# Kernel tuning notes

Hardware: AMD Instinct MI355X
Metric: run time of the kernel (lower is better)

The kernel has to match this reference:

```python
import jax, jax.numpy as jnp
import numpy as np

B, S, D_MODEL, D_Q = 16, 2048, 384, 64


def setup_inputs() -> dict:
    key = jax.random.key(0)
    k1, k2, k3, k4 = jax.random.split(key, 4)
    x = jax.random.normal(k1, (B, S, D_MODEL), dtype=jnp.float32)
    # nn.Linear(d_model, d_q, bias=False) weights, stored as [d_model, d_q] so q = x @ Wq
    scale = 1.0 / np.sqrt(D_MODEL)
    Wq = jax.random.normal(k2, (D_MODEL, D_Q), dtype=jnp.float32) * scale
    Wk = jax.random.normal(k3, (D_MODEL, D_Q), dtype=jnp.float32) * scale
    Wv = jax.random.normal(k4, (D_MODEL, D_Q), dtype=jnp.float32) * scale
    return {"x": x, "Wq": Wq, "Wk": Wk, "Wv": Wv}


def reference(x, Wq, Wk, Wv):
    # x: [B, S, d_model]
    q = jnp.einsum("bsd,de->bse", x, Wq)  # [B, S, d_q]
    k = jnp.einsum("bsd,de->bse", x, Wk)
    v = jnp.einsum("bsd,de->bse", x, Wv)
    d_q = q.shape[-1]
    # full S x S score matrix, scaled by sqrt(d_q) as in the torch code (k.size(-1)**0.5)
    scores = jnp.einsum("bse,bte->bst", q, k) / jnp.sqrt(jnp.float32(d_q))
    s = x.shape[1]
    causal = jnp.tril(jnp.ones((s, s), dtype=bool))  # [S, S]
    scores = jnp.where(causal, scores, jnp.float32(-jnp.inf))
    probs = jax.nn.softmax(scores, axis=-1)
    # dropout is identity in eval/reference mode
    out = jnp.einsum("bst,bte->bse", probs, v)  # [B, S, d_q]
    return out
```

## Files before the change

kernel.cpp:

```cpp
#include <hip/hip_runtime.h>
#include <hip/hip_bf16.h>
#include <math.h>

#define BB 16
#define SS 2048
#define DM 384
#define DQ 64
#define M_ROWS (BB * SS)

typedef short short8 __attribute__((ext_vector_type(8)));
typedef float f32x4  __attribute__((ext_vector_type(4)));
typedef unsigned u32x4 __attribute__((ext_vector_type(4)));

#define WT_OFF 0
#define QB_OFF 73728
#define KB_OFF (QB_OFF + M_ROWS * DQ)
#define VT_OFF (KB_OFF + M_ROWS * DQ)

#define QSCALE 0.18033688011112042f

__device__ __forceinline__ short f2bf(float f) {
  unsigned u = __builtin_bit_cast(unsigned, f);
  unsigned r = (u + 0x7fffu + ((u >> 16) & 1u)) >> 16;
  return (short)r;
}
__device__ __forceinline__ unsigned cvtpk(float a, float b) {
  unsigned r;
  asm("v_cvt_pk_bf16_f32 %0, %1, %2" : "=v"(r) : "v"(a), "v"(b));
  return r;
}
__device__ __forceinline__ void async16(const short* g, short* l) {
  __builtin_amdgcn_global_load_lds(
      (const __attribute__((address_space(1))) unsigned int*)g,
      (__attribute__((address_space(3))) unsigned int*)l, 16, 0, 0);
}

__global__ void prep_w_kernel(const float* __restrict__ Wq,
                              const float* __restrict__ Wk,
                              const float* __restrict__ Wv,
                              short* __restrict__ ws) {
  int o = blockIdx.x * 256 + threadIdx.x;
  int mat = o / (DM * DQ);
  int r = o % (DM * DQ);
  int k = r / DQ, n = r % DQ;
  const float* W = (mat == 0) ? Wq : (mat == 1) ? Wk : Wv;
  ws[WT_OFF + mat * (DM * DQ) + n * DM + k] = f2bf(W[k * DQ + n]);
}

__global__ __launch_bounds__(256) void qkv_proj_mfma(
    const float* __restrict__ x, const short* __restrict__ ws_r,
    short* __restrict__ ws_w) {
  __shared__ short smem[2 * 192 * 64];
  short* Ep = smem;
  const int tid = threadIdx.x;
  const int lane = tid & 63, w = tid >> 6;
  const int cidx = lane & 15, g = lane >> 4;
  const int g8 = g * 8, g4 = g * 4;
  const int sw7 = cidx & 7;
  const int rows0 = blockIdx.x * 64;
  const short* Wt = ws_r + WT_OFF;

  f32x4 acc[12];
  #pragma unroll
  for (int i = 0; i < 12; ++i) acc[i] = (f32x4){0.f, 0.f, 0.f, 0.f};

  const float* xr = x + (size_t)(rows0 + 16 * w + cidx) * DM;

  #pragma unroll
  for (int it = 0; it < 6; ++it) {
    int i = it * 256 + tid;
    int row = i >> 3, gr = i & 7;
    const short* src = Wt + row * DM + ((gr ^ (row & 7)) * 8);
    async16(src, &smem[(it * 256 + w * 64) * 8]);
  }
  float4 xc0 = *(const float4*)(xr + g8);
  float4 xc1 = *(const float4*)(xr + g8 + 4);
  float4 xc2 = *(const float4*)(xr + 32 + g8);
  float4 xc3 = *(const float4*)(xr + 32 + g8 + 4);

  for (int ki = 0; ki < 6; ++ki) {
    __syncthreads();
    const short* cur = smem + (ki & 1) * 12288;

    if (ki < 5) {
      short* nxt = smem + ((ki + 1) & 1) * 12288;
      const int kn = (ki + 1) * 64;
      #pragma unroll
      for (int it = 0; it < 6; ++it) {
        int i = it * 256 + tid;
        int row = i >> 3, gr = i & 7;
        const short* src = Wt + row * DM + kn + ((gr ^ (row & 7)) * 8);
        async16(src, &nxt[(it * 256 + w * 64) * 8]);
      }
    }

    u32x4 ua, ub;
    ua[0] = cvtpk(xc0.x, xc0.y); ua[1] = cvtpk(xc0.z, xc0.w);
    ua[2] = cvtpk(xc1.x, xc1.y); ua[3] = cvtpk(xc1.z, xc1.w);
    ub[0] = cvtpk(xc2.x, xc2.y); ub[1] = cvtpk(xc2.z, xc2.w);
    ub[2] = cvtpk(xc3.x, xc3.y); ub[3] = cvtpk(xc3.z, xc3.w);
    short8 a0 = __builtin_bit_cast(short8, ua);
    short8 a1 = __builtin_bit_cast(short8, ub);

    if (ki < 5) {
      const float* xn = xr + (ki + 1) * 64;
      xc0 = *(const float4*)(xn + g8);
      xc1 = *(const float4*)(xn + g8 + 4);
      xc2 = *(const float4*)(xn + 32 + g8);
      xc3 = *(const float4*)(xn + 32 + g8 + 4);
    }

    #pragma unroll
    for (int ct = 0; ct < 12; ++ct) {
      int row = ct * 16 + cidx;
      short8 b0 = *(const short8*)&cur[row * 64 + ((g ^ sw7) * 8)];
      short8 b1 = *(const short8*)&cur[row * 64 + (((g + 4) ^ sw7) * 8)];
      acc[ct] = __builtin_amdgcn_mfma_f32_16x16x32_bf16(a0, b0, acc[ct], 0, 0, 0);
      acc[ct] = __builtin_amdgcn_mfma_f32_16x16x32_bf16(a1, b1, acc[ct], 0, 0, 0);
    }
  }

  __syncthreads();
  const int erow = 16 * w + g4;
  #pragma unroll
  for (int ct = 0; ct < 4; ++ct) {
    unsigned q01 = cvtpk(acc[ct][0] * QSCALE, acc[ct][1] * QSCALE);
    unsigned q23 = cvtpk(acc[ct][2] * QSCALE, acc[ct][3] * QSCALE);
    unsigned k01 = cvtpk(acc[4 + ct][0], acc[4 + ct][1]);
    unsigned k23 = cvtpk(acc[4 + ct][2], acc[4 + ct][3]);
    unsigned v01 = cvtpk(acc[8 + ct][0], acc[8 + ct][1]);
    unsigned v23 = cvtpk(acc[8 + ct][2], acc[8 + ct][3]);
    Ep[(erow + 0) * 200 + ct * 16 + cidx] = (short)q01;
    Ep[(erow + 1) * 200 + ct * 16 + cidx] = (short)(q01 >> 16);
    Ep[(erow + 2) * 200 + ct * 16 + cidx] = (short)q23;
    Ep[(erow + 3) * 200 + ct * 16 + cidx] = (short)(q23 >> 16);
    Ep[(erow + 0) * 200 + 64 + ct * 16 + cidx] = (short)k01;
    Ep[(erow + 1) * 200 + 64 + ct * 16 + cidx] = (short)(k01 >> 16);
    Ep[(erow + 2) * 200 + 64 + ct * 16 + cidx] = (short)k23;
    Ep[(erow + 3) * 200 + 64 + ct * 16 + cidx] = (short)(k23 >> 16);
    Ep[(ct * 16 + cidx) * 200 + 128 + erow + 0] = (short)v01;
    Ep[(ct * 16 + cidx) * 200 + 128 + erow + 1] = (short)(v01 >> 16);
    Ep[(ct * 16 + cidx) * 200 + 128 + erow + 2] = (short)v23;
    Ep[(ct * 16 + cidx) * 200 + 128 + erow + 3] = (short)(v23 >> 16);
  }
  __syncthreads();

  short* Qb = ws_w + QB_OFF;
  short* Kb = ws_w + KB_OFF;
  short* Vt = ws_w + VT_OFF;
  const int bidx = rows0 >> 11;
  const int srow0 = rows0 & 2047;
  #pragma unroll
  for (int t2 = 0; t2 < 2; ++t2) {
    int i = t2 * 256 + tid;
    int row = i >> 3, gq = i & 7;
    *(short8*)&Qb[(size_t)(rows0 + row) * DQ + gq * 8] =
        *(const short8*)&Ep[row * 200 + gq * 8];
    *(short8*)&Kb[(size_t)(rows0 + row) * DQ + gq * 8] =
        *(const short8*)&Ep[row * 200 + 64 + gq * 8];
    *(short8*)&Vt[(size_t)bidx * (64 * SS) + (size_t)row * SS + srow0 + gq * 8] =
        *(const short8*)&Ep[row * 200 + 128 + gq * 8];
  }
}

__global__ __launch_bounds__(256, 4) void flash_mfma(
    const short* __restrict__ ws, float* __restrict__ O) {
  __shared__ short smem[20480];
  const int b = blockIdx.x;
  const int qx = blockIdx.y;
  const int qt = (b < 8) ? (31 - qx) : qx;
  const int q0 = qt * 64;
  const int tid = threadIdx.x;
  const int lane = tid & 63, w = tid >> 6;
  const int cidx = lane & 15, g = lane >> 4;
  const int g8 = g * 8, g4 = g * 4;
  const int sw7 = cidx & 7;
  short* Ps = smem + 16384 + w * 1024;

  const short* Qb = ws + QB_OFF + (size_t)b * SS * DQ;
  const short* Kb = ws + KB_OFF + (size_t)b * SS * DQ;
  const short* Vt = ws + VT_OFF + (size_t)b * 64 * SS;

  const int qrow = q0 + w * 16;
  const int qglob = qrow + cidx;
  short8 qf0 = *(const short8*)&Qb[(size_t)qglob * DQ + g8];
  short8 qf1 = *(const short8*)&Qb[(size_t)qglob * DQ + 32 + g8];

  const int srow = tid >> 3, sgr = tid & 7;
  const int ssw = (sgr ^ (srow & 7)) * 8;
  const short* kb0 = Kb + (size_t)srow * DQ + ssw;
  const short* kb1 = Kb + (size_t)(srow + 32) * DQ + ssw;
  const short* vb0 = Vt + (size_t)srow * SS + ssw;
  const short* vb1 = Vt + (size_t)(srow + 32) * SS + ssw;
  const int dst0 = (w * 64) * 8, dst1 = (256 + w * 64) * 8;

  f32x4 o[4];
  #pragma unroll
  for (int i = 0; i < 4; ++i) o[i] = (f32x4){0.f, 0.f, 0.f, 0.f};
  float l = 0.f;

  const int nss = qt + 1;

  async16(kb0, &smem[dst0]);
  async16(kb1, &smem[dst1]);
  async16(vb0, &smem[8192 + dst0]);
  async16(vb1, &smem[8192 + dst1]);

  for (int ssi = 0; ssi < nss; ++ssi) {
    __syncthreads();

    {
      int nb = (ssi + 1) * 64;
      if (nb > q0) nb = q0;
      const int nbuf = ((ssi + 1) & 1) * 4096;
      const size_t koff = (size_t)nb * DQ;
      async16(kb0 + koff, &smem[nbuf + dst0]);
      async16(kb1 + koff, &smem[nbuf + dst1]);
      async16(vb0 + nb, &smem[8192 + nbuf + dst0]);
      async16(vb1 + nb, &smem[8192 + nbuf + dst1]);
    }

    const short* Kc = smem + (ssi & 1) * 4096;
    const short* Vc = smem + 8192 + (ssi & 1) * 4096;
    const int kbase = ssi * 64;

    f32x4 sc[4];
    __builtin_amdgcn_s_setprio(1);
    #pragma unroll
    for (int ct = 0; ct < 4; ++ct) {
      int krow = ct * 16 + cidx;
      short8 kf0 = *(const short8*)&Kc[krow * 64 + ((g ^ sw7) * 8)];
      short8 kf1 = *(const short8*)&Kc[krow * 64 + (((g + 4) ^ sw7) * 8)];
      f32x4 a = (f32x4){0.f, 0.f, 0.f, 0.f};
      a = __builtin_amdgcn_mfma_f32_16x16x32_bf16(kf0, qf0, a, 0, 0, 0);
      a = __builtin_amdgcn_mfma_f32_16x16x32_bf16(kf1, qf1, a, 0, 0, 0);
      sc[ct] = a;
    }
    __builtin_amdgcn_s_setprio(0);
    if (ssi == nss - 1) {
      #pragma unroll
      for (int ct = 0; ct < 4; ++ct) {
        int key = kbase + ct * 16 + g4;
        #pragma unroll
        for (int r = 0; r < 4; ++r)
          if (key + r > qglob) sc[ct][r] = -1e30f;
      }
    }
    #pragma unroll
    for (int ct = 0; ct < 4; ++ct) {
      #pragma unroll
      for (int r = 0; r < 4; ++r) {
        float p = __builtin_amdgcn_exp2f(sc[ct][r]);
        sc[ct][r] = p;
        l += p;
      }
      int gb = ct * 2 + (g >> 1);
      uint2 pk;
      pk.x = cvtpk(sc[ct][0], sc[ct][1]);
      pk.y = cvtpk(sc[ct][2], sc[ct][3]);
      *(uint2*)&Ps[cidx * 64 + ((gb ^ sw7) * 8) + (g & 1) * 4] = pk;
    }
    __builtin_amdgcn_s_setprio(1);
    #pragma unroll
    for (int ks = 0; ks < 2; ++ks) {
      short8 pf = *(const short8*)&Ps[cidx * 64 + (((ks * 4 + g) ^ sw7) * 8)];
      #pragma unroll
      for (int dt = 0; dt < 4; ++dt) {
        int vrow = dt * 16 + cidx;
        short8 vf = *(const short8*)&Vc[vrow * 64 + (((ks * 4 + g) ^ sw7) * 8)];
        o[dt] = __builtin_amdgcn_mfma_f32_16x16x32_bf16(vf, pf, o[dt], 0, 0, 0);
      }
    }
    __builtin_amdgcn_s_setprio(0);
  }

  l += __shfl_xor(l, 16);
  l += __shfl_xor(l, 32);
  const float inv = 1.0f / l;

  float* op = O + ((size_t)b * SS + qglob) * DQ;
  #pragma unroll
  for (int dt = 0; dt < 4; ++dt) {
    float4 v = make_float4(o[dt][0] * inv, o[dt][1] * inv,
                           o[dt][2] * inv, o[dt][3] * inv);
    *(float4*)&op[dt * 16 + g4] = v;
  }
}

extern "C" void kernel_launch(void* const* d_in, const int* in_sizes, int n_in,
                              void* d_out, int out_size, void* d_ws, size_t ws_size,
                              hipStream_t stream) {
  const float* x  = (const float*)d_in[0];
  const float* Wq = (const float*)d_in[1];
  const float* Wk = (const float*)d_in[2];
  const float* Wv = (const float*)d_in[3];
  short* ws = (short*)d_ws;
  float* out = (float*)d_out;

  prep_w_kernel<<<288, 256, 0, stream>>>(Wq, Wk, Wv, ws);
  qkv_proj_mfma<<<M_ROWS / 64, 256, 0, stream>>>(x, ws, ws);
  flash_mfma<<<dim3(BB, 32), 256, 0, stream>>>(ws, out);
}
```

Measured before the change: 124.6 us.

## Split causal attention over key ranges and merge partials in a normalize kernel

Each query tile's key range is split into two halves handled by separate blocks, doubling the grid to 1024 blocks with a reordered tile schedule for load balance. Each block writes unnormalized partial outputs and row sums to workspace, and a new kernel adds the halves and divides. The split is exact because no running max is used, so partial exp sums add directly. This aims to improve occupancy and balance across CUs, at the cost of extra global traffic for partials and an additional launch.

```diff
diff --git a/kernel.cpp b/kernel.cpp
--- a/kernel.cpp
+++ b/kernel.cpp
@@ -16,6 +16,8 @@
 #define QB_OFF 73728
 #define KB_OFF (QB_OFF + M_ROWS * DQ)
 #define VT_OFF (KB_OFF + M_ROWS * DQ)
+#define OP_OFF (VT_OFF + BB * DQ * SS)
+#define LS_OFF (OP_OFF + 2 * M_ROWS * DQ * 2)
 
 #define QSCALE 0.18033688011112042f
 
@@ -164,12 +166,21 @@
 }
 
 __global__ __launch_bounds__(256, 4) void flash_mfma(
-    const short* __restrict__ ws, float* __restrict__ O) {
+    const short* __restrict__ ws, float* __restrict__ Op,
+    float* __restrict__ Ls) {
   __shared__ short smem[20480];
-  const int b = blockIdx.x;
-  const int qx = blockIdx.y;
-  const int qt = (b < 8) ? (31 - qx) : qx;
+  const int l = blockIdx.x;
+  const int b = l & 15;
+  const int r = l >> 4;
+  const int qtp = r & 31;
+  const int half = r >> 5;
+  const int qt = (qtp < 16) ? qtp : 47 - qtp;
   const int q0 = qt * 64;
+  const int hsplit = ((qt + 2) >> 1) * 64;
+  const int kstart = half ? hsplit : 0;
+  const int kend = half ? (qt + 1) * 64 : hsplit;
+  const int nss = (kend - kstart) >> 6;
+
   const int tid = threadIdx.x;
   const int lane = tid & 63, w = tid >> 6;
   const int cidx = lane & 15, g = lane >> 4;
@@ -188,103 +199,116 @@
 
   const int srow = tid >> 3, sgr = tid & 7;
   const int ssw = (sgr ^ (srow & 7)) * 8;
-  const short* kb0 = Kb + (size_t)srow * DQ + ssw;
-  const short* kb1 = Kb + (size_t)(srow + 32) * DQ + ssw;
-  const short* vb0 = Vt + (size_t)srow * SS + ssw;
-  const short* vb1 = Vt + (size_t)(srow + 32) * SS + ssw;
+  const short* kb0 = Kb + (size_t)(kstart + srow) * DQ + ssw;
+  const short* kb1 = Kb + (size_t)(kstart + srow + 32) * DQ + ssw;
+  const short* vb0 = Vt + (size_t)srow * SS + kstart + ssw;
+  const short* vb1 = Vt + (size_t)(srow + 32) * SS + kstart + ssw;
   const int dst0 = (w * 64) * 8, dst1 = (256 + w * 64) * 8;
 
   f32x4 o[4];
   #pragma unroll
   for (int i = 0; i < 4; ++i) o[i] = (f32x4){0.f, 0.f, 0.f, 0.f};
-  float l = 0.f;
-
-  const int nss = qt + 1;
-
-  async16(kb0, &smem[dst0]);
-  async16(kb1, &smem[dst1]);
-  async16(vb0, &smem[8192 + dst0]);
-  async16(vb1, &smem[8192 + dst1]);
-
-  for (int ssi = 0; ssi < nss; ++ssi) {
-    __syncthreads();
-
-    {
-      int nb = (ssi + 1) * 64;
-      if (nb > q0) nb = q0;
-      const int nbuf = ((ssi + 1) & 1) * 4096;
-      const size_t koff = (size_t)nb * DQ;
-      async16(kb0 + koff, &smem[nbuf + dst0]);
-      async16(kb1 + koff, &smem[nbuf + dst1]);
-      async16(vb0 + nb, &smem[8192 + nbuf + dst0]);
-      async16(vb1 + nb, &smem[8192 + nbuf + dst1]);
-    }
-
-    const short* Kc = smem + (ssi & 1) * 4096;
-    const short* Vc = smem + 8192 + (ssi & 1) * 4096;
-    const int kbase = ssi * 64;
-
-    f32x4 sc[4];
-    __builtin_amdgcn_s_setprio(1);
-    #pragma unroll
-    for (int ct = 0; ct < 4; ++ct) {
-      int krow = ct * 16 + cidx;
-      short8 kf0 = *(const short8*)&Kc[krow * 64 + ((g ^ sw7) * 8)];
-      short8 kf1 = *(const short8*)&Kc[krow * 64 + (((g + 4) ^ sw7) * 8)];
-      f32x4 a = (f32x4){0.f, 0.f, 0.f, 0.f};
-      a = __builtin_amdgcn_mfma_f32_16x16x32_bf16(kf0, qf0, a, 0, 0, 0);
-      a = __builtin_amdgcn_mfma_f32_16x16x32_bf16(kf1, qf1, a, 0, 0, 0);
-      sc[ct] = a;
-    }
-    __builtin_amdgcn_s_setprio(0);
-    if (ssi == nss - 1) {
+  float lsum = 0.f;
+
+  if (nss > 0) {
+    async16(kb0, &smem[dst0]);
+    async16(kb1, &smem[dst1]);
+    async16(vb0, &smem[8192 + dst0]);
+    async16(vb1, &smem[8192 + dst1]);
+
+    for (int ssi = 0; ssi < nss; ++ssi) {
+      __syncthreads();
+
+      {
+        int nb = (ssi + 1) * 64;
+        if (nb >= kend - kstart) nb = 0;
+        const int nbuf = ((ssi + 1) & 1) * 4096;
+        const size_t koff = (size_t)nb * DQ;
+        async16(kb0 + koff, &smem[nbuf + dst0]);
+        async16(kb1 + koff, &smem[nbuf + dst1]);
+        async16(vb0 + nb, &smem[8192 + nbuf + dst0]);
+        async16(vb1 + nb, &smem[8192 + nbuf + dst1]);
+      }
+
+      const short* Kc = smem + (ssi & 1) * 4096;
+      const short* Vc = smem + 8192 + (ssi & 1) * 4096;
+      const int kbase = kstart + ssi * 64;
+
+      f32x4 sc[4];
+      __builtin_amdgcn_s_setprio(1);
       #pragma unroll
       for (int ct = 0; ct < 4; ++ct) {
-        int key = kbase + ct * 16 + g4;
+        int krow = ct * 16 + cidx;
+        short8 kf0 = *(const short8*)&Kc[krow * 64 + ((g ^ sw7) * 8)];
+        short8 kf1 = *(const short8*)&Kc[krow * 64 + (((g + 4) ^ sw7) * 8)];
+        f32x4 a = (f32x4){0.f, 0.f, 0.f, 0.f};
+        a = __builtin_amdgcn_mfma_f32_16x16x32_bf16(kf0, qf0, a, 0, 0, 0);
+        a = __builtin_amdgcn_mfma_f32_16x16x32_bf16(kf1, qf1, a, 0, 0, 0);
+        sc[ct] = a;
+      }
+      __builtin_amdgcn_s_setprio(0);
+      if (ssi == nss - 1) {
         #pragma unroll
-        for (int r = 0; r < 4; ++r)
-          if (key + r > qglob) sc[ct][r] = -1e30f;
-      }
+        for (int ct = 0; ct < 4; ++ct) {
+          int key = kbase + ct * 16 + g4;
+          #pragma unroll
+          for (int rr = 0; rr < 4; ++rr)
+            if (key + rr > qglob) sc[ct][rr] = -1e30f;
+        }
+      }
+      #pragma unroll
+      for (int ct = 0; ct < 4; ++ct) {
+        #pragma unroll
+        for (int rr = 0; rr < 4; ++rr) {
+          float p = __builtin_amdgcn_exp2f(sc[ct][rr]);
+          sc[ct][rr] = p;
+          lsum += p;
+        }
+        int gb = ct * 2 + (g >> 1);
+        uint2 pk;
+        pk.x = cvtpk(sc[ct][0], sc[ct][1]);
+        pk.y = cvtpk(sc[ct][2], sc[ct][3]);
+        *(uint2*)&Ps[cidx * 64 + ((gb ^ sw7) * 8) + (g & 1) * 4] = pk;
+      }
+      __builtin_amdgcn_s_setprio(1);
+      #pragma unroll
+      for (int ks = 0; ks < 2; ++ks) {
+        short8 pf = *(const short8*)&Ps[cidx * 64 + (((ks * 4 + g) ^ sw7) * 8)];
+        #pragma unroll
+        for (int dt = 0; dt < 4; ++dt) {
+          int vrow = dt * 16 + cidx;
+          short8 vf = *(const short8*)&Vc[vrow * 64 + (((ks * 4 + g) ^ sw7) * 8)];
+          o[dt] = __builtin_amdgcn_mfma_f32_16x16x32_bf16(vf, pf, o[dt], 0, 0, 0);
+        }
+      }
+      __builtin_amdgcn_s_setprio(0);
     }
-    #pragma unroll
-    for (int ct = 0; ct < 4; ++ct) {
-      #pragma unroll
-      for (int r = 0; r < 4; ++r) {
-        float p = __builtin_amdgcn_exp2f(sc[ct][r]);
-        sc[ct][r] = p;
-        l += p;
-      }
-      int gb = ct * 2 + (g >> 1);
-      uint2 pk;
-      pk.x = cvtpk(sc[ct][0], sc[ct][1]);
-      pk.y = cvtpk(sc[ct][2], sc[ct][3]);
-      *(uint2*)&Ps[cidx * 64 + ((gb ^ sw7) * 8) + (g & 1) * 4] = pk;
-    }
-    __builtin_amdgcn_s_setprio(1);
-    #pragma unroll
-    for (int ks = 0; ks < 2; ++ks) {
-      short8 pf = *(const short8*)&Ps[cidx * 64 + (((ks * 4 + g) ^ sw7) * 8)];
-      #pragma unroll
-      for (int dt = 0; dt < 4; ++dt) {
-        int vrow = dt * 16 + cidx;
-        short8 vf = *(const short8*)&Vc[vrow * 64 + (((ks * 4 + g) ^ sw7) * 8)];
-        o[dt] = __builtin_amdgcn_mfma_f32_16x16x32_bf16(vf, pf, o[dt], 0, 0, 0);
-      }
-    }
-    __builtin_amdgcn_s_setprio(0);
-  }
-
-  l += __shfl_xor(l, 16);
-  l += __shfl_xor(l, 32);
-  const float inv = 1.0f / l;
-
-  float* op = O + ((size_t)b * SS + qglob) * DQ;
+  }
+
+  lsum += __shfl_xor(lsum, 16);
+  lsum += __shfl_xor(lsum, 32);
+
+  float* op = Op + (size_t)half * (M_ROWS * DQ) + ((size_t)b * SS + qglob) * DQ;
   #pragma unroll
   for (int dt = 0; dt < 4; ++dt) {
-    float4 v = make_float4(o[dt][0] * inv, o[dt][1] * inv,
-                           o[dt][2] * inv, o[dt][3] * inv);
+    float4 v = make_float4(o[dt][0], o[dt][1], o[dt][2], o[dt][3]);
     *(float4*)&op[dt * 16 + g4] = v;
   }
+  if (g == 0)
+    Ls[(size_t)half * M_ROWS + (size_t)b * SS + qglob] = lsum;
+}
+
+__global__ __launch_bounds__(256) void norm_kernel(
+    const float* __restrict__ Op, const float* __restrict__ Ls,
+    float* __restrict__ O) {
+  int idx = blockIdx.x * 256 + threadIdx.x;
+  int row = idx >> 4, q4 = idx & 15;
+  float li = 1.0f / (Ls[row] + Ls[M_ROWS + row]);
+  float4 a = *(const float4*)&Op[(size_t)row * DQ + q4 * 4];
+  float4 c = *(const float4*)&Op[(size_t)(M_ROWS + row) * DQ + q4 * 4];
+  float4 v = make_float4((a.x + c.x) * li, (a.y + c.y) * li,
+                         (a.z + c.z) * li, (a.w + c.w) * li);
+  *(float4*)&O[(size_t)row * DQ + q4 * 4] = v;
 }
 
 extern "C" void kernel_launch(void* const* d_in, const int* in_sizes, int n_in,
@@ -296,8 +320,11 @@
   const float* Wv = (const float*)d_in[3];
   short* ws = (short*)d_ws;
   float* out = (float*)d_out;
+  float* Op = (float*)(ws + OP_OFF);
+  float* Ls = (float*)(ws + LS_OFF);
 
   prep_w_kernel<<<288, 256, 0, stream>>>(Wq, Wk, Wv, ws);
   qkv_proj_mfma<<<M_ROWS / 64, 256, 0, stream>>>(x, ws, ws);
-  flash_mfma<<<dim3(BB, 32), 256, 0, stream>>>(ws, out);
-}
+  flash_mfma<<<1024, 256, 0, stream>>>(ws, Op, Ls);
+  norm_kernel<<<2048, 256, 0, stream>>>(Op, Ls, out);
+}
```

Measured after the change: 123.3 us (median of 2 runs). About the same (-1.1%).
